# Performance work log

Hardware: AMD Instinct MI355X
Metric: run time of the kernel (lower is better)

## Reference

```python
import math
import jax, jax.numpy as jnp
import numpy as np

H = 16  # num_heads
B, L, D = 1, 256, 1024


def setup_inputs() -> dict:
    key = jax.random.key(0)
    ks = jax.random.split(key, 12)
    s = 1.0 / math.sqrt(D)  # keep activations O(1)
    inp = {
        "mu": jax.random.normal(ks[0], (B, L, D), jnp.float32),
        "var": jax.random.uniform(ks[1], (B, L, D), jnp.float32) + 0.1,
    }
    names = ["q_mu", "q_var", "k_mu", "k_var", "v_mu", "v_var", "o_mu", "o_var"]
    for i, n in enumerate(names):
        inp["w" + n] = jax.random.normal(ks[2 + i], (D, D), jnp.float32) * s
        inp["b" + n] = jnp.zeros((D,), jnp.float32)
    return inp


def _split_heads(x):
    b, l, d = x.shape
    return x.reshape(b, l, H, d // H).transpose(0, 2, 1, 3)  # [B,H,L,Dh]


def _combine_heads(x):
    b, h, l, dh = x.shape
    return x.transpose(0, 2, 1, 3).reshape(b, l, h * dh)


def reference(mu, var, wq_mu, bq_mu, wq_var, bq_var, wk_mu, bk_mu, wk_var, bk_var,
              wv_mu, bv_mu, wv_var, bv_var, wo_mu, bo_mu, wo_var, bo_var):
    dk = mu.shape[-1] // H
    Qm = _split_heads(mu @ wq_mu + bq_mu)
    Qv = _split_heads(jax.nn.softplus(var @ wq_var + bq_var))
    Km = _split_heads(mu @ wk_mu + bk_mu)
    Kv = _split_heads(jax.nn.softplus(var @ wk_var + bk_var))
    Vm = _split_heads(mu @ wv_mu + bv_mu)
    Vv = _split_heads(jax.nn.softplus(var @ wv_var + bv_var))

    # per-element Gaussian KL, broadcast to [B,H,Lq,Lk,Dh] (as in the original)
    diff = (Qm[:, :, :, None, :] - Km[:, :, None, :, :]) ** 2
    ratio = Qv[:, :, :, None, :] / Kv[:, :, None, :, :]
    kl = diff / (2.0 * Kv[:, :, None, :, :]) + 0.5 * (ratio - jnp.log(ratio) - 1.0)
    scores = -kl.sum(-1) * (1.0 / math.sqrt(dk))  # [B,H,Lq,Lk]
    attn = jax.nn.softmax(scores, axis=-1)

    out_mu = jnp.einsum("bhqk,bhkd->bhqd", attn, Vm)
    out_var = jnp.einsum("bhqk,bhkd->bhqd", attn ** 2, Vv)

    O_mu = _combine_heads(out_mu)
    O_var = _combine_heads(out_var)
    mu_out = O_mu @ wo_mu + bo_mu
    var_out = jax.nn.softplus(O_var @ wo_var + bo_var)
    return mu_out, var_out
```

## Files before the change

### kernel.cpp

```cpp
#include <hip/hip_runtime.h>
#include <math.h>

typedef __bf16 bf16_t;
typedef bf16_t bf16x4 __attribute__((ext_vector_type(4)));
typedef bf16_t bf16x8 __attribute__((ext_vector_type(8)));
typedef float  f32x4  __attribute__((ext_vector_type(4)));

__device__ __forceinline__ float softplus_f(float x) {
    return (x > 20.f) ? x : log1pf(expf(x));
}

__device__ __forceinline__ float fast_rcp(float x) {
#if __has_builtin(__builtin_amdgcn_rcpf)
    return __builtin_amdgcn_rcpf(x);
#else
    return 1.0f / x;
#endif
}

struct PrepArgs { const float* src[8]; };

__global__ __launch_bounds__(256) void prep_kernel(PrepArgs pa, bf16_t* __restrict__ wtbase) {
    const int t = threadIdx.x;
    const int kt = blockIdx.x, nt = blockIdx.y, wm = blockIdx.z;
    const float* __restrict__ W = pa.src[wm];
    bf16_t* __restrict__ Wt = wtbase + (size_t)wm * 1048576;
    __shared__ bf16_t Ts[64][72];
    const int r0 = t >> 4, c4 = (t & 15) * 4;
#pragma unroll
    for (int rep = 0; rep < 4; ++rep) {
        const int r = r0 + rep * 16;
        const float4 v = *(const float4*)&W[(size_t)(kt * 64 + r) * 1024 + nt * 64 + c4];
        Ts[c4 + 0][r] = (bf16_t)v.x;
        Ts[c4 + 1][r] = (bf16_t)v.y;
        Ts[c4 + 2][r] = (bf16_t)v.z;
        Ts[c4 + 3][r] = (bf16_t)v.w;
    }
    __syncthreads();
#pragma unroll
    for (int rep = 0; rep < 2; ++rep) {
        const int chunk = t + rep * 256;
        const int n = chunk >> 3, kc = (chunk & 7) * 8;
        bf16x8 v = *(const bf16x8*)&Ts[n][kc];
        *(bf16x8*)&Wt[(size_t)(nt * 64 + n) * 1024 + kt * 64 + kc] = v;
    }
}

template<bool AF32>
__device__ __forceinline__ void gemm4_core(const void* Aptr, const bf16_t* __restrict__ Wt,
                                           const int m_base, const int n_base,
                                           unsigned char* smem, const int t, f32x4 out[4]) {
    __syncthreads();
    bf16_t* stage = (bf16_t*)smem;
    float*  Cr    = (float*)smem;
    const int lane = t & 63, w = t >> 6;
    bf16_t* As = stage + w * 9216;
    bf16_t* Bs = As + 4608;
    const int r8 = lane >> 3, kb = lane & 7;
    const int fr = lane & 15, fq = lane >> 4, fk = fq * 8;

    const bf16_t* Bb = Wt + (size_t)n_base * 1024 + w * 256 + kb * 8;
    const float*  Af = (const float*)Aptr  + (size_t)m_base * 1024 + w * 256 + kb * 8;
    const bf16_t* Ab = (const bf16_t*)Aptr + (size_t)m_base * 1024 + w * 256 + kb * 8;

    f32x4 acc[4][4] = {};
    bf16x8 pa[8], pb[8];
    f32x4 paf0[8], paf1[8];
#pragma unroll
    for (int i = 0; i < 8; ++i) {
        pb[i] = *(const bf16x8*)(Bb + (size_t)(i * 8 + r8) * 1024);
        if constexpr (AF32) {
            paf0[i] = *(const f32x4*)(Af + (size_t)(i * 8 + r8) * 1024);
            paf1[i] = *(const f32x4*)(Af + (size_t)(i * 8 + r8) * 1024 + 4);
        } else {
            pa[i] = *(const bf16x8*)(Ab + (size_t)(i * 8 + r8) * 1024);
        }
    }

#pragma unroll
    for (int s = 0; s < 4; ++s) {
#pragma unroll
        for (int i = 0; i < 8; ++i) {
            bf16x8 av;
            if constexpr (AF32) {
#pragma unroll
                for (int e = 0; e < 4; ++e) {
                    av[e]     = (bf16_t)paf0[i][e];
                    av[e + 4] = (bf16_t)paf1[i][e];
                }
            } else {
                av = pa[i];
            }
            *(bf16x8*)&As[(i * 8 + r8) * 72 + kb * 8] = av;
            *(bf16x8*)&Bs[(i * 8 + r8) * 72 + kb * 8] = pb[i];
        }
        if (s < 3) {
            const int off = (s + 1) * 64;
#pragma unroll
            for (int i = 0; i < 8; ++i) {
                pb[i] = *(const bf16x8*)(Bb + (size_t)(i * 8 + r8) * 1024 + off);
                if constexpr (AF32) {
                    paf0[i] = *(const f32x4*)(Af + (size_t)(i * 8 + r8) * 1024 + off);
                    paf1[i] = *(const f32x4*)(Af + (size_t)(i * 8 + r8) * 1024 + off + 4);
                } else {
                    pa[i] = *(const bf16x8*)(Ab + (size_t)(i * 8 + r8) * 1024 + off);
                }
            }
        }
#pragma unroll
        for (int kh = 0; kh < 2; ++kh) {
            bf16x8 aF[4], bF[4];
#pragma unroll
            for (int i = 0; i < 4; ++i)
                aF[i] = *(const bf16x8*)&As[(i * 16 + fr) * 72 + kh * 32 + fk];
#pragma unroll
            for (int j = 0; j < 4; ++j)
                bF[j] = *(const bf16x8*)&Bs[(j * 16 + fr) * 72 + kh * 32 + fk];
#pragma unroll
            for (int i = 0; i < 4; ++i)
#pragma unroll
                for (int j = 0; j < 4; ++j)
                    acc[i][j] = __builtin_amdgcn_mfma_f32_16x16x32_bf16(aF[i], bF[j], acc[i][j], 0, 0, 0);
        }
    }

    __syncthreads();
    {
        float* Crw = Cr + w * 4352;
        const int orow = fq * 4;
#pragma unroll
        for (int i = 0; i < 4; ++i)
#pragma unroll
            for (int j = 0; j < 4; ++j)
#pragma unroll
                for (int rr = 0; rr < 4; ++rr)
                    Crw[(i * 16 + orow + rr) * 68 + j * 16 + fr] = acc[i][j][rr];
    }
    __syncthreads();

    const int cc = (t & 15) * 4;
#pragma unroll
    for (int i = 0; i < 4; ++i) {
        const int row = (t >> 4) + i * 16;
        f32x4 s0 = *(const f32x4*)&Cr[0 * 4352 + row * 68 + cc];
        f32x4 s1 = *(const f32x4*)&Cr[1 * 4352 + row * 68 + cc];
        f32x4 s2 = *(const f32x4*)&Cr[2 * 4352 + row * 68 + cc];
        f32x4 s3 = *(const f32x4*)&Cr[3 * 4352 + row * 68 + cc];
        out[i] = (s0 + s1) + (s2 + s3);
    }
}

struct ProjArgs {
    const float* mu; const float* var;
    const bf16_t* WtB;
    const float* bias[6];
    float* Proj;
    bf16_t* Gbf; float* cvec;
};

__global__ __launch_bounds__(256, 2) void proj_kernel(ProjArgs a) {
    __shared__ __align__(16) unsigned char smem[73728];
    const int z = blockIdx.z;
    const int nb = blockIdx.x * 64, mb = blockIdx.y * 64;
    const int t = threadIdx.x;
    const int cc = (t & 15) * 4;

    if (z != 2) {
        const int wi   = (z < 2) ? z : (z + 1);
        const int slot = (z < 2) ? z : (z - 1);
        const int sp   = (z == 1) || (z == 4);
        const void* A  = (z == 1 || z == 4) ? (const void*)a.var : (const void*)a.mu;
        f32x4 o[4];
        gemm4_core<true>(A, a.WtB + (size_t)wi * 1048576, mb, nb, smem, t, o);
        const f32x4 bv = *(const f32x4*)&a.bias[wi][nb + cc];
        float* dst = a.Proj + (size_t)slot * 262144;
#pragma unroll
        for (int i = 0; i < 4; ++i) {
            const int row = (t >> 4) + i * 16;
            f32x4 v = o[i] + bv;
            if (sp) {
                v[0] = softplus_f(v[0]); v[1] = softplus_f(v[1]);
                v[2] = softplus_f(v[2]); v[3] = softplus_f(v[3]);
            }
            *(f32x4*)&dst[(size_t)(mb + row) * 1024 + nb + cc] = v;
        }
    } else {
        const int h = blockIdx.x;
        f32x4 okm[4], okv[4];
        gemm4_core<true>(a.mu,  a.WtB + (size_t)2 * 1048576, mb, nb, smem, t, okm);
        gemm4_core<true>(a.var, a.WtB + (size_t)3 * 1048576, mb, nb, smem, t, okv);
        const f32x4 bkm = *(const f32x4*)&a.bias[2][nb + cc];
        const f32x4 bkv = *(const f32x4*)&a.bias[3][nb + cc];
#pragma unroll
        for (int i = 0; i < 4; ++i) {
            const int row = (t >> 4) + i * 16;
            const int katt = mb + row;
            const f32x4 km  = okm[i] + bkm;
            const f32x4 kvr = okv[i] + bkv;
            bf16x4 o1, o2;
            float c = 0.f;
#pragma unroll
            for (int e = 0; e < 4; ++e) {
                const float kv = softplus_f(kvr[e]);
                const float r  = 0.5f * fast_rcp(kv);
                o1[e] = (bf16_t)r;
                o2[e] = (bf16_t)(-2.f * km[e] * r);
                c += km[e] * km[e] * r + 0.5f * __logf(kv);
            }
            bf16_t* grow = a.Gbf + ((size_t)(h * 256 + katt)) * 128;
            *(bf16x4*)&grow[cc]      = o1;
            *(bf16x4*)&grow[64 + cc] = o2;
#pragma unroll
            for (int off = 8; off > 0; off >>= 1)
                c += __shfl_xor(c, off, 16);
            if ((t & 15) == 0)
                a.cvec[h * 256 + katt] = c;
        }
    }
}

#define OFF_VM   0
#define OFF_VV   36864
#define OFF_FS   73728
#define OFF_SC   82176
#define OFF_PHI  98816
#define OFF_PLO  107264
#define OFF_P2H  115712
#define OFF_P2L  124160
#define ATTN_SMEM 132608

__global__ __launch_bounds__(512) void attn_v7(const float* __restrict__ Qm,
                                               const float* __restrict__ Qv,
                                               const bf16_t* __restrict__ Gbf,
                                               const float* __restrict__ cvec,
                                               const float* __restrict__ Vm,
                                               const float* __restrict__ Vv,
                                               bf16_t* __restrict__ Omu,
                                               bf16_t* __restrict__ Ovar) {
    __shared__ __align__(16) unsigned char smem[ATTN_SMEM];
    bf16_t* Vsm = (bf16_t*)(smem + OFF_VM);
    bf16_t* Vsv = (bf16_t*)(smem + OFF_VV);
    float*  Fs  = (float*)(smem + OFF_FS);
    float*  Sc  = (float*)(smem + OFF_SC);
    bf16_t* Phi = (bf16_t*)(smem + OFF_PHI);
    bf16_t* Plo = (bf16_t*)(smem + OFF_PLO);
    bf16_t* P2h = (bf16_t*)(smem + OFF_P2H);
    bf16_t* P2l = (bf16_t*)(smem + OFF_P2L);

    const int qt = blockIdx.x, h = blockIdx.y;
    const int t = threadIdx.x, w = t >> 6, lane = t & 63;
    const int fr = lane & 15, fq = lane >> 4;
    const int n0 = w * 32;

    const bf16_t* gB = Gbf + ((size_t)(h * 256 + n0 + fr)) * 128 + fq * 8;

    bf16x8 bcur[4];
#pragma unroll
    for (int ks = 0; ks < 4; ++ks) bcur[ks] = *(const bf16x8*)(gB + ks * 32);

    if (t < 256) {
        const int r = t >> 4, c = t & 15;
        f32x4 qm = *(const f32x4*)(Qm + (size_t)(qt * 16 + r) * 1024 + h * 64 + c * 4);
        f32x4 qv = *(const f32x4*)(Qv + (size_t)(qt * 16 + r) * 1024 + h * 64 + c * 4);
        *(f32x4*)&Fs[r * 132 + c * 4]      = qm * qm + qv;
        *(f32x4*)&Fs[r * 132 + 64 + c * 4] = qm;
    }
    __syncthreads();

    bf16x8 ahi[4], alo[4];
#pragma unroll
    for (int ks = 0; ks < 4; ++ks) {
        f32x4 f0 = *(const f32x4*)&Fs[fr * 132 + ks * 32 + fq * 8];
        f32x4 f1 = *(const f32x4*)&Fs[fr * 132 + ks * 32 + fq * 8 + 4];
#pragma unroll
        for (int e = 0; e < 4; ++e) {
            bf16_t hb = (bf16_t)f0[e];
            ahi[ks][e] = hb; alo[ks][e] = (bf16_t)(f0[e] - (float)hb);
            bf16_t hb2 = (bf16_t)f1[e];
            ahi[ks][e + 4] = hb2; alo[ks][e + 4] = (bf16_t)(f1[e] - (float)hb2);
        }
    }

    const int tm = t & 255;
    const int vk = tm >> 2, vpart = tm & 3;
    const float* Vsrc = (t >= 256) ? Vv : Vm;
    bf16_t*      Vdst = (t >= 256) ? Vsv : Vsm;

#pragma unroll
    for (int nt = 0; nt < 2; ++nt) {
        const int ra = vk + (2 * nt) * 64;
        const int rb = vk + (2 * nt + 1) * 64;
        const float* vsa = Vsrc + (size_t)ra * 1024 + h * 64 + vpart * 16;
        const float* vsb = Vsrc + (size_t)rb * 1024 + h * 64 + vpart * 16;
        f32x4 va0 = *(const f32x4*)(vsa),     va1 = *(const f32x4*)(vsa + 4);
        f32x4 va2 = *(const f32x4*)(vsa + 8), va3 = *(const f32x4*)(vsa + 12);
        f32x4 vb0 = *(const f32x4*)(vsb),     vb1 = *(const f32x4*)(vsb + 4);
        f32x4 vb2 = *(const f32x4*)(vsb + 8), vb3 = *(const f32x4*)(vsb + 12);

        bf16x8 bnxt[4];
        if (nt < 1) {
#pragma unroll
            for (int ks = 0; ks < 4; ++ks)
                bnxt[ks] = *(const bf16x8*)(gB + 2048 + ks * 32);
        }

        f32x4 acc = {0.f, 0.f, 0.f, 0.f};
#pragma unroll
        for (int ks = 0; ks < 4; ++ks) {
            acc = __builtin_amdgcn_mfma_f32_16x16x32_bf16(ahi[ks], bcur[ks], acc, 0, 0, 0);
            acc = __builtin_amdgcn_mfma_f32_16x16x32_bf16(alo[ks], bcur[ks], acc, 0, 0, 0);
        }

        {
            bf16_t* da = Vdst + ra * 72 + vpart * 16;
            bf16_t* db = Vdst + rb * 72 + vpart * 16;
            bf16x8 o0, o1;
            o0[0]=(bf16_t)va0[0]; o0[1]=(bf16_t)va0[1]; o0[2]=(bf16_t)va0[2]; o0[3]=(bf16_t)va0[3];
            o0[4]=(bf16_t)va1[0]; o0[5]=(bf16_t)va1[1]; o0[6]=(bf16_t)va1[2]; o0[7]=(bf16_t)va1[3];
            o1[0]=(bf16_t)va2[0]; o1[1]=(bf16_t)va2[1]; o1[2]=(bf16_t)va2[2]; o1[3]=(bf16_t)va2[3];
            o1[4]=(bf16_t)va3[0]; o1[5]=(bf16_t)va3[1]; o1[6]=(bf16_t)va3[2]; o1[7]=(bf16_t)va3[3];
            *(bf16x8*)(da)     = o0;
            *(bf16x8*)(da + 8) = o1;
            o0[0]=(bf16_t)vb0[0]; o0[1]=(bf16_t)vb0[1]; o0[2]=(bf16_t)vb0[2]; o0[3]=(bf16_t)vb0[3];
            o0[4]=(bf16_t)vb1[0]; o0[5]=(bf16_t)vb1[1]; o0[6]=(bf16_t)vb1[2]; o0[7]=(bf16_t)vb1[3];
            o1[0]=(bf16_t)vb2[0]; o1[1]=(bf16_t)vb2[1]; o1[2]=(bf16_t)vb2[2]; o1[3]=(bf16_t)vb2[3];
            o1[4]=(bf16_t)vb3[0]; o1[5]=(bf16_t)vb3[1]; o1[6]=(bf16_t)vb3[2]; o1[7]=(bf16_t)vb3[3];
            *(bf16x8*)(db)     = o0;
            *(bf16x8*)(db + 8) = o1;
        }

        const float cv = cvec[h * 256 + n0 + nt * 16 + fr];
        f32x4 lg = (acc + cv) * (-0.125f);
#pragma unroll
        for (int reg = 0; reg < 4; ++reg)
            Sc[(fq * 4 + reg) * 260 + n0 + nt * 16 + fr] = lg[reg];

#pragma unroll
        for (int ks = 0; ks < 4; ++ks) bcur[ks] = bnxt[ks];
    }
    __syncthreads();

    const int fw = w * 2;
    f32x4 sr[2];
#pragma unroll
    for (int r = 0; r < 2; ++r)
        sr[r] = *(const f32x4*)&Sc[(fw + r) * 260 + lane * 4];
#pragma unroll
    for (int r = 0; r < 2; ++r) {
        f32x4 s = sr[r];
        float mloc = fmaxf(fmaxf(s[0], s[1]), fmaxf(s[2], s[3]));
#pragma unroll
        for (int off = 32; off > 0; off >>= 1)
            mloc = fmaxf(mloc, __shfl_xor(mloc, off, 64));
        s[0] = __expf(s[0] - mloc); s[1] = __expf(s[1] - mloc);
        s[2] = __expf(s[2] - mloc); s[3] = __expf(s[3] - mloc);
        float sl = (s[0] + s[1]) + (s[2] + s[3]);
#pragma unroll
        for (int off = 32; off > 0; off >>= 1)
            sl += __shfl_xor(sl, off, 64);
        sr[r] = s * fast_rcp(sl);
    }

#pragma unroll
    for (int r = 0; r < 2; ++r) {
        bf16x4 phi, plo, p2hi, p2lo;
#pragma unroll
        for (int e = 0; e < 4; ++e) {
            const float p = sr[r][e];
            const bf16_t hb = (bf16_t)p;
            phi[e] = hb; plo[e] = (bf16_t)(p - (float)hb);
            const float p2 = p * p;
            const bf16_t h2 = (bf16_t)p2;
            p2hi[e] = h2; p2lo[e] = (bf16_t)(p2 - (float)h2);
        }
        const int row = fw + r;
        *(bf16x4*)&Phi[row * 264 + lane * 4] = phi;
        *(bf16x4*)&Plo[row * 264 + lane * 4] = plo;
        *(bf16x4*)&P2h[row * 264 + lane * 4] = p2hi;
        *(bf16x4*)&P2l[row * 264 + lane * 4] = p2lo;
    }
    __syncthreads();

    const int tile = w & 3;
    const int isvar = w >> 2;
    const bf16_t* Pa = isvar ? P2h : Phi;
    const bf16_t* Pb = isvar ? P2l : Plo;
    const bf16_t* Vs = isvar ? Vsv : Vsm;
    f32x4 accp = {0.f, 0.f, 0.f, 0.f};
#pragma unroll
    for (int k0 = 0; k0 < 256; k0 += 32) {
        const int ka = k0 + fq * 8;
        bf16x8 a1 = *(const bf16x8*)&Pa[fr * 264 + ka];
        bf16x8 a2 = *(const bf16x8*)&Pb[fr * 264 + ka];
        bf16x8 bfr;
#pragma unroll
        for (int j = 0; j < 8; ++j)
            bfr[j] = Vs[(ka + j) * 72 + tile * 16 + fr];
        accp = __builtin_amdgcn_mfma_f32_16x16x32_bf16(a1, bfr, accp, 0, 0, 0);
        accp = __builtin_amdgcn_mfma_f32_16x16x32_bf16(a2, bfr, accp, 0, 0, 0);
    }

    bf16_t* Out = isvar ? Ovar : Omu;
#pragma unroll
    for (int reg = 0; reg < 4; ++reg) {
        const int qg = qt * 16 + fq * 4 + reg;
        const size_t ob = (size_t)qg * 1024 + h * 64 + tile * 16 + fr;
        Out[ob] = (bf16_t)accp[reg];
    }
}

struct OutArgs {
    const bf16_t* A[2];
    const bf16_t* Wt[2];
    const float*  bias[2];
    float*        dst[2];
    int           splus[2];
};

__global__ __launch_bounds__(256, 2) void out_gemm(OutArgs args) {
    const int z = blockIdx.z;
    const bf16_t* __restrict__ A    = args.A[z];
    const bf16_t* __restrict__ Wt   = args.Wt[z];
    const float*  __restrict__ bias = args.bias[z];
    float*        __restrict__ dst  = args.dst[z];
    const int sp = args.splus[z];

    const int n_base = blockIdx.x * 64;
    const int m_base = blockIdx.y * 64;

    __shared__ __align__(16) unsigned char smem[73728];
    const int t = threadIdx.x;
    f32x4 o[4];
    gemm4_core<false>(A, Wt, m_base, n_base, smem, t, o);

    const int cc = (t & 15) * 4;
    const f32x4 bv = *(const f32x4*)&bias[n_base + cc];
#pragma unroll
    for (int i = 0; i < 4; ++i) {
        const int row = (t >> 4) + i * 16;
        f32x4 v = o[i] + bv;
        if (sp) {
            v[0] = softplus_f(v[0]); v[1] = softplus_f(v[1]);
            v[2] = softplus_f(v[2]); v[3] = softplus_f(v[3]);
        }
        *(f32x4*)&dst[(size_t)(m_base + row) * 1024 + n_base + cc] = v;
    }
}

extern "C" void kernel_launch(void* const* d_in, const int* in_sizes, int n_in,
                              void* d_out, int out_size, void* d_ws, size_t ws_size,
                              hipStream_t stream) {
    const float* mu  = (const float*)d_in[0];
    const float* var = (const float*)d_in[1];
    uint8_t* ws = (uint8_t*)d_ws;

    bf16_t* WtB  = (bf16_t*)(ws);
    float*  Proj = (float*)(ws + (16u << 20));
    bf16_t* Obm  = (bf16_t*)(ws + (20u << 20));
    bf16_t* Obv  = (bf16_t*)(ws + (20u << 20) + (512u << 10));
    bf16_t* Gbf  = (bf16_t*)(ws + (21u << 20));
    float*  cvec = (float*)(ws + (22u << 20));

    PrepArgs pa;
    for (int i = 0; i < 8; ++i) pa.src[i] = (const float*)d_in[2 + 2 * i];
    prep_kernel<<<dim3(16, 16, 8), 256, 0, stream>>>(pa, WtB);

    ProjArgs pr;
    pr.mu = mu; pr.var = var; pr.WtB = WtB;
    for (int i = 0; i < 6; ++i) pr.bias[i] = (const float*)d_in[3 + 2 * i];
    pr.Proj = Proj; pr.Gbf = Gbf; pr.cvec = cvec;
    proj_kernel<<<dim3(16, 4, 5), 256, 0, stream>>>(pr);

    attn_v7<<<dim3(16, 16), 512, 0, stream>>>(Proj, Proj + 262144, Gbf, cvec,
                                              Proj + 2 * 262144, Proj + 3 * 262144,
                                              Obm, Obv);

    OutArgs g3;
    g3.A[0] = Obm;  g3.Wt[0] = WtB + (size_t)6 * 1048576;
    g3.bias[0] = (const float*)d_in[15];
    g3.dst[0] = (float*)d_out;             g3.splus[0] = 0;
    g3.A[1] = Obv;  g3.Wt[1] = WtB + (size_t)7 * 1048576;
    g3.bias[1] = (const float*)d_in[17];
    g3.dst[1] = (float*)d_out + 262144;    g3.splus[1] = 1;
    out_gemm<<<dim3(16, 4, 2), 256, 0, stream>>>(g3);
}
```

Before: 150.8 us.

## Fuse weight bf16 conversion and transpose into GEMM tile loads, drop prep kernel

Removes the separate prep kernel that converted all eight fp32 weight matrices to transposed bf16 in workspace. The GEMM core now loads fp32 weights directly in their original [K,N] layout, converts them to bf16 in registers and writes them transposed into shared memory. This saves one launch and a full read/write pass over 32 MB of weights. In exchange each GEMM block reads twice as many weight bytes, uses more registers for the prefetch buffers, and does scattered transposed LDS stores.

```diff
diff --git a/kernel.cpp b/kernel.cpp
--- a/kernel.cpp
+++ b/kernel.cpp
@@ -18,36 +18,8 @@
 #endif
 }
 
-struct PrepArgs { const float* src[8]; };
-
-__global__ __launch_bounds__(256) void prep_kernel(PrepArgs pa, bf16_t* __restrict__ wtbase) {
-    const int t = threadIdx.x;
-    const int kt = blockIdx.x, nt = blockIdx.y, wm = blockIdx.z;
-    const float* __restrict__ W = pa.src[wm];
-    bf16_t* __restrict__ Wt = wtbase + (size_t)wm * 1048576;
-    __shared__ bf16_t Ts[64][72];
-    const int r0 = t >> 4, c4 = (t & 15) * 4;
-#pragma unroll
-    for (int rep = 0; rep < 4; ++rep) {
-        const int r = r0 + rep * 16;
-        const float4 v = *(const float4*)&W[(size_t)(kt * 64 + r) * 1024 + nt * 64 + c4];
-        Ts[c4 + 0][r] = (bf16_t)v.x;
-        Ts[c4 + 1][r] = (bf16_t)v.y;
-        Ts[c4 + 2][r] = (bf16_t)v.z;
-        Ts[c4 + 3][r] = (bf16_t)v.w;
-    }
-    __syncthreads();
-#pragma unroll
-    for (int rep = 0; rep < 2; ++rep) {
-        const int chunk = t + rep * 256;
-        const int n = chunk >> 3, kc = (chunk & 7) * 8;
-        bf16x8 v = *(const bf16x8*)&Ts[n][kc];
-        *(bf16x8*)&Wt[(size_t)(nt * 64 + n) * 1024 + kt * 64 + kc] = v;
-    }
-}
-
 template<bool AF32>
-__device__ __forceinline__ void gemm4_core(const void* Aptr, const bf16_t* __restrict__ Wt,
+__device__ __forceinline__ void gemmT_core(const void* Aptr, const float* __restrict__ Wf,
                                            const int m_base, const int n_base,
                                            unsigned char* smem, const int t, f32x4 out[4]) {
     __syncthreads();
@@ -58,17 +30,20 @@
     bf16_t* Bs = As + 4608;
     const int r8 = lane >> 3, kb = lane & 7;
     const int fr = lane & 15, fq = lane >> 4, fk = fq * 8;
-
-    const bf16_t* Bb = Wt + (size_t)n_base * 1024 + w * 256 + kb * 8;
+    const int bc = fr;
+    const int br16 = fq * 16;
+
     const float*  Af = (const float*)Aptr  + (size_t)m_base * 1024 + w * 256 + kb * 8;
     const bf16_t* Ab = (const bf16_t*)Aptr + (size_t)m_base * 1024 + w * 256 + kb * 8;
+    const float*  Bf = Wf + (size_t)(w * 256 + br16) * 1024 + n_base + bc * 4;
 
     f32x4 acc[4][4] = {};
-    bf16x8 pa[8], pb[8];
+    bf16x8 pa[8];
     f32x4 paf0[8], paf1[8];
+    f32x4 pbf[16];
+
 #pragma unroll
     for (int i = 0; i < 8; ++i) {
-        pb[i] = *(const bf16x8*)(Bb + (size_t)(i * 8 + r8) * 1024);
         if constexpr (AF32) {
             paf0[i] = *(const f32x4*)(Af + (size_t)(i * 8 + r8) * 1024);
             paf1[i] = *(const f32x4*)(Af + (size_t)(i * 8 + r8) * 1024 + 4);
@@ -76,6 +51,9 @@
             pa[i] = *(const bf16x8*)(Ab + (size_t)(i * 8 + r8) * 1024);
         }
     }
+#pragma unroll
+    for (int i = 0; i < 16; ++i)
+        pbf[i] = *(const f32x4*)(Bf + (size_t)i * 1024);
 
 #pragma unroll
     for (int s = 0; s < 4; ++s) {
@@ -92,13 +70,22 @@
                 av = pa[i];
             }
             *(bf16x8*)&As[(i * 8 + r8) * 72 + kb * 8] = av;
-            *(bf16x8*)&Bs[(i * 8 + r8) * 72 + kb * 8] = pb[i];
+        }
+#pragma unroll
+        for (int e = 0; e < 4; ++e) {
+            bf16x8 lo, hi;
+#pragma unroll
+            for (int q = 0; q < 8; ++q) {
+                lo[q] = (bf16_t)pbf[q][e];
+                hi[q] = (bf16_t)pbf[q + 8][e];
+            }
+            *(bf16x8*)&Bs[(bc * 4 + e) * 72 + br16]     = lo;
+            *(bf16x8*)&Bs[(bc * 4 + e) * 72 + br16 + 8] = hi;
         }
         if (s < 3) {
             const int off = (s + 1) * 64;
 #pragma unroll
             for (int i = 0; i < 8; ++i) {
-                pb[i] = *(const bf16x8*)(Bb + (size_t)(i * 8 + r8) * 1024 + off);
                 if constexpr (AF32) {
                     paf0[i] = *(const f32x4*)(Af + (size_t)(i * 8 + r8) * 1024 + off);
                     paf1[i] = *(const f32x4*)(Af + (size_t)(i * 8 + r8) * 1024 + off + 4);
@@ -106,6 +93,9 @@
                     pa[i] = *(const bf16x8*)(Ab + (size_t)(i * 8 + r8) * 1024 + off);
                 }
             }
+#pragma unroll
+            for (int i = 0; i < 16; ++i)
+                pbf[i] = *(const f32x4*)(Bf + (size_t)i * 1024 + (size_t)off * 1024);
         }
 #pragma unroll
         for (int kh = 0; kh < 2; ++kh) {
@@ -152,7 +142,7 @@
 
 struct ProjArgs {
     const float* mu; const float* var;
-    const bf16_t* WtB;
+    const float* W[6];
     const float* bias[6];
     float* Proj;
     bf16_t* Gbf; float* cvec;
@@ -171,7 +161,7 @@
         const int sp   = (z == 1) || (z == 4);
         const void* A  = (z == 1 || z == 4) ? (const void*)a.var : (const void*)a.mu;
         f32x4 o[4];
-        gemm4_core<true>(A, a.WtB + (size_t)wi * 1048576, mb, nb, smem, t, o);
+        gemmT_core<true>(A, a.W[wi], mb, nb, smem, t, o);
         const f32x4 bv = *(const f32x4*)&a.bias[wi][nb + cc];
         float* dst = a.Proj + (size_t)slot * 262144;
 #pragma unroll
@@ -187,8 +177,8 @@
     } else {
         const int h = blockIdx.x;
         f32x4 okm[4], okv[4];
-        gemm4_core<true>(a.mu,  a.WtB + (size_t)2 * 1048576, mb, nb, smem, t, okm);
-        gemm4_core<true>(a.var, a.WtB + (size_t)3 * 1048576, mb, nb, smem, t, okv);
+        gemmT_core<true>(a.mu,  a.W[2], mb, nb, smem, t, okm);
+        gemmT_core<true>(a.var, a.W[3], mb, nb, smem, t, okv);
         const f32x4 bkm = *(const f32x4*)&a.bias[2][nb + cc];
         const f32x4 bkv = *(const f32x4*)&a.bias[3][nb + cc];
 #pragma unroll
@@ -411,7 +401,7 @@
 
 struct OutArgs {
     const bf16_t* A[2];
-    const bf16_t* Wt[2];
+    const float*  W[2];
     const float*  bias[2];
     float*        dst[2];
     int           splus[2];
@@ -420,7 +410,7 @@
 __global__ __launch_bounds__(256, 2) void out_gemm(OutArgs args) {
     const int z = blockIdx.z;
     const bf16_t* __restrict__ A    = args.A[z];
-    const bf16_t* __restrict__ Wt   = args.Wt[z];
+    const float*  __restrict__ W    = args.W[z];
     const float*  __restrict__ bias = args.bias[z];
     float*        __restrict__ dst  = args.dst[z];
     const int sp = args.splus[z];
@@ -431,7 +421,7 @@
     __shared__ __align__(16) unsigned char smem[73728];
     const int t = threadIdx.x;
     f32x4 o[4];
-    gemm4_core<false>(A, Wt, m_base, n_base, smem, t, o);
+    gemmT_core<false>(A, W, m_base, n_base, smem, t, o);
 
     const int cc = (t & 15) * 4;
     const f32x4 bv = *(const f32x4*)&bias[n_base + cc];
@@ -454,20 +444,18 @@
     const float* var = (const float*)d_in[1];
     uint8_t* ws = (uint8_t*)d_ws;
 
-    bf16_t* WtB  = (bf16_t*)(ws);
-    float*  Proj = (float*)(ws + (16u << 20));
-    bf16_t* Obm  = (bf16_t*)(ws + (20u << 20));
-    bf16_t* Obv  = (bf16_t*)(ws + (20u << 20) + (512u << 10));
-    bf16_t* Gbf  = (bf16_t*)(ws + (21u << 20));
-    float*  cvec = (float*)(ws + (22u << 20));
-
-    PrepArgs pa;
-    for (int i = 0; i < 8; ++i) pa.src[i] = (const float*)d_in[2 + 2 * i];
-    prep_kernel<<<dim3(16, 16, 8), 256, 0, stream>>>(pa, WtB);
+    float*  Proj = (float*)(ws);
+    bf16_t* Obm  = (bf16_t*)(ws + (4u << 20));
+    bf16_t* Obv  = (bf16_t*)(ws + (4u << 20) + (512u << 10));
+    bf16_t* Gbf  = (bf16_t*)(ws + (5u << 20));
+    float*  cvec = (float*)(ws + (6u << 20));
 
     ProjArgs pr;
-    pr.mu = mu; pr.var = var; pr.WtB = WtB;
-    for (int i = 0; i < 6; ++i) pr.bias[i] = (const float*)d_in[3 + 2 * i];
+    pr.mu = mu; pr.var = var;
+    for (int i = 0; i < 6; ++i) {
+        pr.W[i]    = (const float*)d_in[2 + 2 * i];
+        pr.bias[i] = (const float*)d_in[3 + 2 * i];
+    }
     pr.Proj = Proj; pr.Gbf = Gbf; pr.cvec = cvec;
     proj_kernel<<<dim3(16, 4, 5), 256, 0, stream>>>(pr);
 
@@ -476,10 +464,10 @@
                                               Obm, Obv);
 
     OutArgs g3;
-    g3.A[0] = Obm;  g3.Wt[0] = WtB + (size_t)6 * 1048576;
+    g3.A[0] = Obm;  g3.W[0] = (const float*)d_in[14];
     g3.bias[0] = (const float*)d_in[15];
     g3.dst[0] = (float*)d_out;             g3.splus[0] = 0;
-    g3.A[1] = Obv;  g3.Wt[1] = WtB + (size_t)7 * 1048576;
+    g3.A[1] = Obv;  g3.W[1] = (const float*)d_in[16];
     g3.bias[1] = (const float*)d_in[17];
     g3.dst[1] = (float*)d_out + 262144;    g3.splus[1] = 1;
     out_gemm<<<dim3(16, 4, 2), 256, 0, stream>>>(g3);
```

New measurement: 148.5 us. Within noise of the previous version (-1.5%).
